# Optimization experiments

Measured on AMD Instinct MI355X. Metric: run time of the kernel, lower is better.

Reference implementation:

```python
import jax, jax.numpy as jnp
import numpy as np

B, T, I, H = 256, 512, 64, 256


def _lstm_layer(x, Wih, Whh, bih, bhh):
    # x: [B, T, in], Wih: [4H, in], Whh: [4H, H], biases: [4H]
    # PyTorch gate order: i, f, g, o.  c' = f*c + i*g ; h = o*tanh(c')
    Hd = Whh.shape[1]
    xp = jnp.einsum('bti,gi->btg', x, Wih) + bih + bhh  # [B, T, 4H]
    h0 = jnp.zeros((x.shape[0], Hd), x.dtype)
    c0 = jnp.zeros((x.shape[0], Hd), x.dtype)

    def step(carry, xt):
        h, c = carry
        g = xt + h @ Whh.T
        i, f, gg, o = jnp.split(g, 4, axis=-1)
        i = jax.nn.sigmoid(i)
        f = jax.nn.sigmoid(f)
        gg = jnp.tanh(gg)
        o = jax.nn.sigmoid(o)
        c = f * c + i * gg
        h = o * jnp.tanh(c)
        return (h, c), h

    _, hs = jax.lax.scan(step, (h0, c0), jnp.swapaxes(xp, 0, 1))  # [T, B, H]
    return jnp.swapaxes(hs, 0, 1)


def setup_inputs() -> dict:
    key = jax.random.key(0)
    ks = jax.random.split(key, 20)
    s_in = 1.0 / np.sqrt(I)
    s_h = 1.0 / np.sqrt(H)
    d = {
        'x': jax.random.normal(ks[0], (B, T, I), jnp.float32),
        # encoder layer 0: input I -> H
        'enc_Wih0': jax.random.normal(ks[1], (4 * H, I), jnp.float32) * s_in,
        'enc_Whh0': jax.random.normal(ks[2], (4 * H, H), jnp.float32) * s_h,
        'enc_bih0': jnp.zeros((4 * H,), jnp.float32),
        'enc_bhh0': jnp.zeros((4 * H,), jnp.float32),
        # encoder layer 1: H -> H
        'enc_Wih1': jax.random.normal(ks[3], (4 * H, H), jnp.float32) * s_h,
        'enc_Whh1': jax.random.normal(ks[4], (4 * H, H), jnp.float32) * s_h,
        'enc_bih1': jnp.zeros((4 * H,), jnp.float32),
        'enc_bhh1': jnp.zeros((4 * H,), jnp.float32),
        # decoder layer 0: H -> H
        'dec_Wih0': jax.random.normal(ks[5], (4 * H, H), jnp.float32) * s_h,
        'dec_Whh0': jax.random.normal(ks[6], (4 * H, H), jnp.float32) * s_h,
        'dec_bih0': jnp.zeros((4 * H,), jnp.float32),
        'dec_bhh0': jnp.zeros((4 * H,), jnp.float32),
        # decoder layer 1: H -> H
        'dec_Wih1': jax.random.normal(ks[7], (4 * H, H), jnp.float32) * s_h,
        'dec_Whh1': jax.random.normal(ks[8], (4 * H, H), jnp.float32) * s_h,
        'dec_bih1': jnp.zeros((4 * H,), jnp.float32),
        'dec_bhh1': jnp.zeros((4 * H,), jnp.float32),
        # output projection H -> I
        'out_W': jax.random.normal(ks[9], (I, H), jnp.float32) * s_h,
        'out_b': jnp.zeros((I,), jnp.float32),
    }
    return d


def reference(x,
              enc_Wih0, enc_Whh0, enc_bih0, enc_bhh0,
              enc_Wih1, enc_Whh1, enc_bih1, enc_bhh1,
              dec_Wih0, dec_Whh0, dec_bih0, dec_bhh0,
              dec_Wih1, dec_Whh1, dec_bih1, dec_bhh1,
              out_W, out_b):
    # Encoder (2 stacked LSTM layers, inference mode -> no inter-layer dropout)
    h = _lstm_layer(x, enc_Wih0, enc_Whh0, enc_bih0, enc_bhh0)
    encoded = _lstm_layer(h, enc_Wih1, enc_Whh1, enc_bih1, enc_bhh1)
    # Decoder (2 stacked LSTM layers over the encoded sequence)
    h = _lstm_layer(encoded, dec_Wih0, dec_Whh0, dec_bih0, dec_bhh0)
    decoded_hidden = _lstm_layer(h, dec_Wih1, dec_Whh1, dec_bih1, dec_bhh1)
    # Linear projection back to input_size
    reconstruction = jnp.einsum('bth,ih->bti', decoded_hidden, out_W) + out_b
    return reconstruction
```

## Files before the change

### kernel.cpp

```cpp
#include <hip/hip_runtime.h>

typedef unsigned short u16;
typedef unsigned int   u32;
typedef _Float16 f16;
typedef _Float16 half2v __attribute__((ext_vector_type(2)));
typedef _Float16 half8v __attribute__((ext_vector_type(8)));
typedef float float4v __attribute__((ext_vector_type(4)));

#define B_  256
#define T_  512
#define I_  64
#define H_  256
#define G_  1024
#define BT_ (B_*T_)

static __device__ __forceinline__ float fdot2u(u32 a, u32 b, float c) {
#if defined(__has_builtin) && __has_builtin(__builtin_amdgcn_fdot2)
  return __builtin_amdgcn_fdot2(__builtin_bit_cast(half2v, a),
                                __builtin_bit_cast(half2v, b), c, false);
#else
  half2v av = __builtin_bit_cast(half2v, a), bv = __builtin_bit_cast(half2v, b);
  return c + (float)av.x * (float)bv.x + (float)av.y * (float)bv.y;
#endif
}

static __device__ __forceinline__ float sig_(float x) {
  return 1.0f / (1.0f + __expf(-x));
}
static __device__ __forceinline__ float tanh_(float x) {
  float ax = fminf(fabsf(x), 15.0f);
  float e  = __expf(2.0f * ax);
  float t  = (e - 1.0f) / (e + 1.0f);
  return copysignf(t, x);
}


__global__ void cvt_f16(const float* __restrict__ in, u16* __restrict__ out, int n) {
  int i = blockIdx.x * blockDim.x + threadIdx.x;
  if (i < n) out[i] = __builtin_bit_cast(u16, (f16)in[i]);
}

__global__ void split_w(const float* __restrict__ w, u16* __restrict__ hi,
                        u16* __restrict__ lo, int n) {
  int i = blockIdx.x * blockDim.x + threadIdx.x;
  if (i < n) {
    float v = w[i];
    f16 h = (f16)v;
    float r = v - (float)h;
    hi[i] = __builtin_bit_cast(u16, h);
    lo[i] = __builtin_bit_cast(u16, (f16)r);
  }
}

__global__ void bias_sum(const float* __restrict__ a, const float* __restrict__ b,
                         float* __restrict__ o, int n) {
  int i = blockIdx.x * blockDim.x + threadIdx.x;
  if (i < n) o[i] = a[i] + b[i];
}

template<int BN>
__global__ __launch_bounds__(256) void gemm_ws(
    const u16* __restrict__ A, const u16* __restrict__ Bh, const u16* __restrict__ Bl,
    const float* __restrict__ bias, float* __restrict__ C,
    int K, int tcl, int t0, int N)
{
  constexpr int BM = 128, BK = 64, LDT = 72;
  __shared__ u16 As[BM * LDT];
  __shared__ u16 Bhs[BN * LDT];
  __shared__ u16 Bls[BN * LDT];
  const int tid = threadIdx.x, wave = tid >> 6, lane = tid & 63;
  const int m0 = blockIdx.x * BM, n0 = blockIdx.y * BN;
  constexpr int WNT = BN / 32;
  const int wm0 = (wave >> 1) * 64, wn0 = (wave & 1) * (BN / 2);
  const int tcmask = (1 << tcl) - 1;
  float4v acc[4][WNT];
  for (int i = 0; i < 4; i++)
    for (int j = 0; j < WNT; j++) acc[i][j] = (float4v){0.f, 0.f, 0.f, 0.f};
  const int lrow = lane & 15, lk = (lane >> 4) * 8;

  for (int k0 = 0; k0 < K; k0 += BK) {
    __syncthreads();
#pragma unroll
    for (int i = 0; i < 4; i++) {
      int idx = tid + i * 256, row = idx >> 3, u = idx & 7;
      int m = m0 + row;
      int rg = (m >> tcl) * T_ + t0 + (m & tcmask);
      *(uint4*)(As + row * LDT + u * 8) =
          *(const uint4*)(A + (size_t)rg * K + k0 + u * 8);
    }
#pragma unroll
    for (int i = 0; i < WNT; i++) {
      int idx = tid + i * 256, row = idx >> 3, u = idx & 7;
      size_t go = (size_t)(n0 + row) * K + k0 + u * 8;
      *(uint4*)(Bhs + row * LDT + u * 8) = *(const uint4*)(Bh + go);
      *(uint4*)(Bls + row * LDT + u * 8) = *(const uint4*)(Bl + go);
    }
    __syncthreads();
#pragma unroll
    for (int ks = 0; ks < 2; ++ks) {
      int col = ks * 32 + lk;
      half8v af[4];
#pragma unroll
      for (int mt = 0; mt < 4; mt++)
        af[mt] = *(const half8v*)(const void*)(As + (wm0 + mt * 16 + lrow) * LDT + col);
#pragma unroll
      for (int nt = 0; nt < WNT; nt++) {
        half8v bhv = *(const half8v*)(const void*)(Bhs + (wn0 + nt * 16 + lrow) * LDT + col);
        half8v blv = *(const half8v*)(const void*)(Bls + (wn0 + nt * 16 + lrow) * LDT + col);
#pragma unroll
        for (int mt = 0; mt < 4; mt++) {
          acc[mt][nt] = __builtin_amdgcn_mfma_f32_16x16x32_f16(af[mt], bhv, acc[mt][nt], 0, 0, 0);
          acc[mt][nt] = __builtin_amdgcn_mfma_f32_16x16x32_f16(af[mt], blv, acc[mt][nt], 0, 0, 0);
        }
      }
    }
  }
  const int crow = (lane >> 4) * 4, ccol = lane & 15;
#pragma unroll
  for (int nt = 0; nt < WNT; nt++) {
    int n = n0 + wn0 + nt * 16 + ccol;
    float bv = bias[n];
#pragma unroll
    for (int mt = 0; mt < 4; mt++) {
#pragma unroll
      for (int r = 0; r < 4; r++) {
        int m = m0 + wm0 + mt * 16 + crow + r;
        C[(size_t)m * N + n] = acc[mt][nt][r] + bv;
      }
    }
  }
}

__global__ __launch_bounds__(512) __attribute__((amdgpu_waves_per_eu(2, 2)))
void lstm_scan(
    const u16* __restrict__ whh, const float* __restrict__ xp,
    u16* __restrict__ hout, float* __restrict__ cst, u16* __restrict__ hst,
    int Tc, int t0)
{
  __shared__ u16 wt[8 * 1024 * 8];
  __shared__ u32 hbuf[2][128];
  const int tid = threadIdx.x, b = blockIdx.x;
  const int lane = tid & 63, wv = tid >> 6;
  const int u = wv * 32 + (lane & 31);
  const int g0 = lane >> 5;
  const int r0 = g0 * 256 + u;
  const int r1 = (g0 + 2) * 256 + u;

  uint4 w0[24], w1[24];
  {
    const uint4* gp0 = (const uint4*)(whh + (size_t)r0 * 256);
    const uint4* gp1 = (const uint4*)(whh + (size_t)r1 * 256);
#pragma unroll
    for (int i = 0; i < 24; i++) { w0[i] = gp0[i]; w1[i] = gp1[i]; }
#pragma unroll
    for (int q = 0; q < 8; q++) {
      *(uint4*)(wt + (size_t)(q * 1024 + r0) * 8) = gp0[24 + q];
      *(uint4*)(wt + (size_t)(q * 1024 + r1) * 8) = gp1[24 + q];
    }
  }

  float cc = 0.f;
  if (t0 == 0) {
    if (tid < 128) hbuf[0][tid] = 0u;
  } else {
    cc = cst[(size_t)b * 256 + u];
    if (tid < 128) hbuf[0][tid] = ((const u32*)hst)[(size_t)b * 128 + tid];
  }
  __syncthreads();

  const float* xpb = xp + (size_t)b * Tc * 1024;
  float xn0 = xpb[r0], xn1 = xpb[r1];
  u16* houtb = hout + ((size_t)b * T_ + t0) * 256;

  u16 hb = 0;
  for (int tt = 0; tt < Tc; ++tt) {
    float a0 = xn0, a1 = xn1;
    if (tt + 1 < Tc) {
      xn0 = xpb[(size_t)(tt + 1) * 1024 + r0];
      xn1 = xpb[(size_t)(tt + 1) * 1024 + r1];
    }
    const uint4* hq = (const uint4*)hbuf[tt & 1];
#pragma unroll
    for (int kc = 0; kc < 24; ++kc) {
      uint4 hv = hq[kc];
      a0 = fdot2u(w0[kc].x, hv.x, a0); a0 = fdot2u(w0[kc].y, hv.y, a0);
      a0 = fdot2u(w0[kc].z, hv.z, a0); a0 = fdot2u(w0[kc].w, hv.w, a0);
      a1 = fdot2u(w1[kc].x, hv.x, a1); a1 = fdot2u(w1[kc].y, hv.y, a1);
      a1 = fdot2u(w1[kc].z, hv.z, a1); a1 = fdot2u(w1[kc].w, hv.w, a1);
    }
#pragma unroll
    for (int q = 0; q < 8; ++q) {
      uint4 hv = hq[24 + q];
      uint4 t0v = *(const uint4*)(wt + (size_t)(q * 1024 + r0) * 8);
      uint4 t1v = *(const uint4*)(wt + (size_t)(q * 1024 + r1) * 8);
      a0 = fdot2u(t0v.x, hv.x, a0); a0 = fdot2u(t0v.y, hv.y, a0);
      a0 = fdot2u(t0v.z, hv.z, a0); a0 = fdot2u(t0v.w, hv.w, a0);
      a1 = fdot2u(t1v.x, hv.x, a1); a1 = fdot2u(t1v.y, hv.y, a1);
      a1 = fdot2u(t1v.z, hv.z, a1); a1 = fdot2u(t1v.w, hv.w, a1);
    }
    float b0 = __shfl_xor(a0, 32);
    float b1 = __shfl_xor(a1, 32);
    float ipre = g0 ? b0 : a0;
    float fpre = g0 ? a0 : b0;
    float gpre = g0 ? b1 : a1;
    float opre = g0 ? a1 : b1;
    float iv = sig_(ipre), fv = sig_(fpre), gv = tanh_(gpre), ov = sig_(opre);
    cc = fv * cc + iv * gv;
    float hval = ov * tanh_(cc);
    hb = __builtin_bit_cast(u16, (f16)hval);
    if (g0 == 0) {
      ((u16*)hbuf[(tt + 1) & 1])[u] = hb;
      houtb[(size_t)tt * 256 + u] = hb;
    }
    __syncthreads();
  }
  if (g0 == 0) {
    cst[(size_t)b * 256 + u] = cc;
    hst[(size_t)b * 256 + u] = hb;
  }
}


extern "C" void kernel_launch(void* const* d_in, const int* in_sizes, int n_in,
                              void* d_out, int out_size, void* d_ws, size_t ws_size,
                              hipStream_t stream)
{
  const float* x      = (const float*)d_in[0];
  const float* Wih[4] = {(const float*)d_in[1], (const float*)d_in[5],
                         (const float*)d_in[9], (const float*)d_in[13]};
  const float* Whh[4] = {(const float*)d_in[2], (const float*)d_in[6],
                         (const float*)d_in[10], (const float*)d_in[14]};
  const float* bi[4]  = {(const float*)d_in[3], (const float*)d_in[7],
                         (const float*)d_in[11], (const float*)d_in[15]};
  const float* bh[4]  = {(const float*)d_in[4], (const float*)d_in[8],
                         (const float*)d_in[12], (const float*)d_in[16]};
  const float* outW   = (const float*)d_in[17];
  const float* outb   = (const float*)d_in[18];

  char* ws = (char*)d_ws;
  size_t off = 0;
  auto alc = [&](size_t bytes) -> char* {
    char* p = ws + off;
    off = (off + bytes + 255) & ~(size_t)255;
    return p;
  };

  u16* xf  = (u16*)alc((size_t)BT_ * I_ * 2);
  u16* hb0 = (u16*)alc((size_t)BT_ * H_ * 2);
  u16* hb1 = (u16*)alc((size_t)BT_ * H_ * 2);
  int wihn[4] = {G_ * I_, G_ * H_, G_ * H_, G_ * H_};
  u16 *wihH[4], *wihL[4], *whhH[4];
  float* bsum[4];
  for (int l = 0; l < 4; l++) {
    wihH[l] = (u16*)alc((size_t)wihn[l] * 2);
    wihL[l] = (u16*)alc((size_t)wihn[l] * 2);
    whhH[l] = (u16*)alc((size_t)G_ * H_ * 2);
    bsum[l] = (float*)alc((size_t)G_ * 4);
  }
  u16* owH = (u16*)alc((size_t)I_ * H_ * 2);
  u16* owL = (u16*)alc((size_t)I_ * H_ * 2);
  float* cst = (float*)alc((size_t)B_ * H_ * 4);
  u16*   hst = (u16*)alc((size_t)B_ * H_ * 2);

  int Tc = T_;
  while (Tc > 16 && off + (size_t)B_ * Tc * G_ * 4 + 4096 > ws_size) Tc >>= 1;
  float* xpb = (float*)alc((size_t)B_ * Tc * G_ * 4);
  int tcl = 0;
  while ((1 << tcl) < Tc) tcl++;

  {
    int n = BT_ * I_;
    cvt_f16<<<dim3((n + 255) / 256), dim3(256), 0, stream>>>(x, xf, n);
  }
  for (int l = 0; l < 4; l++) {
    split_w<<<dim3((wihn[l] + 255) / 256), dim3(256), 0, stream>>>(Wih[l], wihH[l], wihL[l], wihn[l]);
    cvt_f16<<<dim3((G_ * H_ + 255) / 256), dim3(256), 0, stream>>>(Whh[l], whhH[l], G_ * H_);
    bias_sum<<<dim3(4), dim3(256), 0, stream>>>(bi[l], bh[l], bsum[l], G_);
  }
  split_w<<<dim3((I_ * H_ + 255) / 256), dim3(256), 0, stream>>>(outW, owH, owL, I_ * H_);

  for (int l = 0; l < 4; l++) {
    const u16* Ain = (l == 0) ? xf : ((l == 1) ? hb0 : (l == 2) ? hb1 : hb0);
    u16* Hout = (l & 1) ? hb1 : hb0;
    int K = (l == 0) ? I_ : H_;
    for (int t0 = 0; t0 < T_; t0 += Tc) {
      gemm_ws<128><<<dim3((B_ * Tc) / 128, G_ / 128), dim3(256), 0, stream>>>(
          Ain, wihH[l], wihL[l], bsum[l], xpb, K, tcl, t0, G_);
      lstm_scan<<<dim3(B_), dim3(512), 0, stream>>>(whhH[l], xpb, Hout, cst, hst, Tc, t0);
    }
  }

  gemm_ws<64><<<dim3(BT_ / 128, 1), dim3(256), 0, stream>>>(
      hb1, owH, owL, outb, (float*)d_out, H_, 9, 0, I_);
}
```

Measured before the change: 5.279 ms.

## Pin recurrent weights in AGPRs and broadcast hidden state via readlane

Stores the register-resident W_hh slice in accumulation registers (AGPRs) through inline-asm pinning and copies it back to VGPRs at use. This frees VGPRs and drops the waves_per_eu constraint. For the first 16 chunks, the hidden state is loaded once per lane and broadcast with readlane instead of repeated LDS vector loads, which cuts LDS traffic on the serial recurrence. The cost is extra AGPR-to-VGPR moves and scalar readlane instructions on every timestep, and the inline-asm constraints may not steer register allocation as intended.

```diff
diff --git a/kernel.cpp b/kernel.cpp
--- a/kernel.cpp
+++ b/kernel.cpp
@@ -13,6 +13,9 @@
 #define H_  256
 #define G_  1024
 #define BT_ (B_*T_)
+
+#define AG_PIN(dst, src) asm volatile("" : "=a"(dst) : "0"(src))
+#define AG_GET(dst, src) asm volatile("" : "=v"(dst) : "0"(src))
 
 static __device__ __forceinline__ float fdot2u(u32 a, u32 b, float c) {
 #if defined(__has_builtin) && __has_builtin(__builtin_amdgcn_fdot2)
@@ -131,8 +134,7 @@
   }
 }
 
-__global__ __launch_bounds__(512) __attribute__((amdgpu_waves_per_eu(2, 2)))
-void lstm_scan(
+__global__ __launch_bounds__(512) void lstm_scan(
     const u16* __restrict__ whh, const float* __restrict__ xp,
     u16* __restrict__ hout, float* __restrict__ cst, u16* __restrict__ hst,
     int Tc, int t0)
@@ -146,12 +148,16 @@
   const int r0 = g0 * 256 + u;
   const int r1 = (g0 + 2) * 256 + u;
 
-  uint4 w0[24], w1[24];
+  float4v wA[48];
   {
     const uint4* gp0 = (const uint4*)(whh + (size_t)r0 * 256);
     const uint4* gp1 = (const uint4*)(whh + (size_t)r1 * 256);
 #pragma unroll
-    for (int i = 0; i < 24; i++) { w0[i] = gp0[i]; w1[i] = gp1[i]; }
+    for (int i = 0; i < 24; i++) {
+      uint4 q0 = gp0[i], q1 = gp1[i];
+      AG_PIN(wA[i],      __builtin_bit_cast(float4v, q0));
+      AG_PIN(wA[24 + i], __builtin_bit_cast(float4v, q1));
+    }
 #pragma unroll
     for (int q = 0; q < 8; q++) {
       *(uint4*)(wt + (size_t)(q * 1024 + r0) * 8) = gp0[24 + q];
@@ -179,14 +185,38 @@
       xn0 = xpb[(size_t)(tt + 1) * 1024 + r0];
       xn1 = xpb[(size_t)(tt + 1) * 1024 + r1];
     }
-    const uint4* hq = (const uint4*)hbuf[tt & 1];
-#pragma unroll
-    for (int kc = 0; kc < 24; ++kc) {
+    const u32* hcur = hbuf[tt & 1];
+    u32 hg = hcur[lane];
+    const uint4* hq = (const uint4*)hcur;
+
+#pragma unroll
+    for (int kc = 0; kc < 16; ++kc) {
+      float4v q0, q1;
+      AG_GET(q0, wA[kc]);
+      AG_GET(q1, wA[24 + kc]);
+      uint4 w0 = __builtin_bit_cast(uint4, q0);
+      uint4 w1 = __builtin_bit_cast(uint4, q1);
+      u32 h0 = __builtin_amdgcn_readlane(hg, 4 * kc + 0);
+      u32 h1 = __builtin_amdgcn_readlane(hg, 4 * kc + 1);
+      u32 h2 = __builtin_amdgcn_readlane(hg, 4 * kc + 2);
+      u32 h3 = __builtin_amdgcn_readlane(hg, 4 * kc + 3);
+      a0 = fdot2u(w0.x, h0, a0); a0 = fdot2u(w0.y, h1, a0);
+      a0 = fdot2u(w0.z, h2, a0); a0 = fdot2u(w0.w, h3, a0);
+      a1 = fdot2u(w1.x, h0, a1); a1 = fdot2u(w1.y, h1, a1);
+      a1 = fdot2u(w1.z, h2, a1); a1 = fdot2u(w1.w, h3, a1);
+    }
+#pragma unroll
+    for (int kc = 16; kc < 24; ++kc) {
+      float4v q0, q1;
+      AG_GET(q0, wA[kc]);
+      AG_GET(q1, wA[24 + kc]);
+      uint4 w0 = __builtin_bit_cast(uint4, q0);
+      uint4 w1 = __builtin_bit_cast(uint4, q1);
       uint4 hv = hq[kc];
-      a0 = fdot2u(w0[kc].x, hv.x, a0); a0 = fdot2u(w0[kc].y, hv.y, a0);
-      a0 = fdot2u(w0[kc].z, hv.z, a0); a0 = fdot2u(w0[kc].w, hv.w, a0);
-      a1 = fdot2u(w1[kc].x, hv.x, a1); a1 = fdot2u(w1[kc].y, hv.y, a1);
-      a1 = fdot2u(w1[kc].z, hv.z, a1); a1 = fdot2u(w1[kc].w, hv.w, a1);
+      a0 = fdot2u(w0.x, hv.x, a0); a0 = fdot2u(w0.y, hv.y, a0);
+      a0 = fdot2u(w0.z, hv.z, a0); a0 = fdot2u(w0.w, hv.w, a0);
+      a1 = fdot2u(w1.x, hv.x, a1); a1 = fdot2u(w1.y, hv.y, a1);
+      a1 = fdot2u(w1.z, hv.z, a1); a1 = fdot2u(w1.w, hv.w, a1);
     }
 #pragma unroll
     for (int q = 0; q < 8; ++q) {
```

New measurement: 7.700 ms. 45.9% more time.

## Broadcast hidden state via readlane and move one more weight chunk to LDS

Applied to the files above, without the earlier changes.

The recurrent matvec in the LSTM scan no longer reads the hidden state from LDS as uint4 broadcasts each step. Instead each wave loads the 128 packed h words into two VGPRs and broadcasts them to scalar registers with readlane. One more 16-byte weight chunk per row moves from registers to LDS (23 in registers, 9 in LDS), which lowers register pressure. The main loop is marked not to unroll, and the xp prefetch is made unconditional by clamping the index. The aim is to cut LDS read traffic and free registers, at the cost of many readlane/SALU instructions and extra LDS weight reads on the critical serial path.

```diff
diff --git a/kernel.cpp b/kernel.cpp
--- a/kernel.cpp
+++ b/kernel.cpp
@@ -131,13 +131,14 @@
   }
 }
 
-__global__ __launch_bounds__(512) __attribute__((amdgpu_waves_per_eu(2, 2)))
+__global__ __attribute__((amdgpu_flat_work_group_size(512, 512),
+                          amdgpu_waves_per_eu(2, 2)))
 void lstm_scan(
     const u16* __restrict__ whh, const float* __restrict__ xp,
     u16* __restrict__ hout, float* __restrict__ cst, u16* __restrict__ hst,
     int Tc, int t0)
 {
-  __shared__ u16 wt[8 * 1024 * 8];
+  __shared__ u16 wt[9 * 1024 * 8];
   __shared__ u32 hbuf[2][128];
   const int tid = threadIdx.x, b = blockIdx.x;
   const int lane = tid & 63, wv = tid >> 6;
@@ -146,25 +147,29 @@
   const int r0 = g0 * 256 + u;
   const int r1 = (g0 + 2) * 256 + u;
 
-  uint4 w0[24], w1[24];
   {
     const uint4* gp0 = (const uint4*)(whh + (size_t)r0 * 256);
     const uint4* gp1 = (const uint4*)(whh + (size_t)r1 * 256);
 #pragma unroll
-    for (int i = 0; i < 24; i++) { w0[i] = gp0[i]; w1[i] = gp1[i]; }
-#pragma unroll
-    for (int q = 0; q < 8; q++) {
-      *(uint4*)(wt + (size_t)(q * 1024 + r0) * 8) = gp0[24 + q];
-      *(uint4*)(wt + (size_t)(q * 1024 + r1) * 8) = gp1[24 + q];
-    }
-  }
-
+    for (int q = 0; q < 9; q++) {
+      *(uint4*)(wt + (q * 1024 + r0) * 8) = gp0[23 + q];
+      *(uint4*)(wt + (q * 1024 + r1) * 8) = gp1[23 + q];
+    }
+  }
   float cc = 0.f;
   if (t0 == 0) {
     if (tid < 128) hbuf[0][tid] = 0u;
   } else {
-    cc = cst[(size_t)b * 256 + u];
-    if (tid < 128) hbuf[0][tid] = ((const u32*)hst)[(size_t)b * 128 + tid];
+    cc = cst[b * 256 + u];
+    if (tid < 128) hbuf[0][tid] = ((const u32*)hst)[b * 128 + tid];
+  }
+
+  uint4 wr0[23], wr1[23];
+  {
+    const uint4* gp0 = (const uint4*)(whh + (size_t)r0 * 256);
+    const uint4* gp1 = (const uint4*)(whh + (size_t)r1 * 256);
+#pragma unroll
+    for (int i = 0; i < 23; i++) { wr0[i] = gp0[i]; wr1[i] = gp1[i]; }
   }
   __syncthreads();
 
@@ -173,30 +178,44 @@
   u16* houtb = hout + ((size_t)b * T_ + t0) * 256;
 
   u16 hb = 0;
+#pragma clang loop unroll(disable)
   for (int tt = 0; tt < Tc; ++tt) {
     float a0 = xn0, a1 = xn1;
-    if (tt + 1 < Tc) {
-      xn0 = xpb[(size_t)(tt + 1) * 1024 + r0];
-      xn1 = xpb[(size_t)(tt + 1) * 1024 + r1];
-    }
-    const uint4* hq = (const uint4*)hbuf[tt & 1];
-#pragma unroll
-    for (int kc = 0; kc < 24; ++kc) {
-      uint4 hv = hq[kc];
-      a0 = fdot2u(w0[kc].x, hv.x, a0); a0 = fdot2u(w0[kc].y, hv.y, a0);
-      a0 = fdot2u(w0[kc].z, hv.z, a0); a0 = fdot2u(w0[kc].w, hv.w, a0);
-      a1 = fdot2u(w1[kc].x, hv.x, a1); a1 = fdot2u(w1[kc].y, hv.y, a1);
-      a1 = fdot2u(w1[kc].z, hv.z, a1); a1 = fdot2u(w1[kc].w, hv.w, a1);
-    }
-#pragma unroll
-    for (int q = 0; q < 8; ++q) {
-      uint4 hv = hq[24 + q];
-      uint4 t0v = *(const uint4*)(wt + (size_t)(q * 1024 + r0) * 8);
-      uint4 t1v = *(const uint4*)(wt + (size_t)(q * 1024 + r1) * 8);
-      a0 = fdot2u(t0v.x, hv.x, a0); a0 = fdot2u(t0v.y, hv.y, a0);
-      a0 = fdot2u(t0v.z, hv.z, a0); a0 = fdot2u(t0v.w, hv.w, a0);
-      a1 = fdot2u(t1v.x, hv.x, a1); a1 = fdot2u(t1v.y, hv.y, a1);
-      a1 = fdot2u(t1v.z, hv.z, a1); a1 = fdot2u(t1v.w, hv.w, a1);
+    {
+      int ttn = (tt + 1 < Tc) ? (tt + 1) : tt;
+      xn0 = xpb[ttn * 1024 + r0];
+      xn1 = xpb[ttn * 1024 + r1];
+    }
+    const u32* hcur = hbuf[tt & 1];
+    u32 hg0 = hcur[lane];
+    u32 hg1 = hcur[64 + lane];
+
+#pragma unroll
+    for (int qi = 0; qi < 32; ++qi) {
+      u32 h0, h1, h2, h3;
+      if (qi < 16) {
+        h0 = __builtin_amdgcn_readlane(hg0, 4 * qi + 0);
+        h1 = __builtin_amdgcn_readlane(hg0, 4 * qi + 1);
+        h2 = __builtin_amdgcn_readlane(hg0, 4 * qi + 2);
+        h3 = __builtin_amdgcn_readlane(hg0, 4 * qi + 3);
+      } else {
+        h0 = __builtin_amdgcn_readlane(hg1, 4 * qi - 64);
+        h1 = __builtin_amdgcn_readlane(hg1, 4 * qi - 63);
+        h2 = __builtin_amdgcn_readlane(hg1, 4 * qi - 62);
+        h3 = __builtin_amdgcn_readlane(hg1, 4 * qi - 61);
+      }
+      uint4 w0, w1;
+      if (qi < 23) {
+        w0 = wr0[qi];
+        w1 = wr1[qi];
+      } else {
+        w0 = *(const uint4*)(wt + ((qi - 23) * 1024 + r0) * 8);
+        w1 = *(const uint4*)(wt + ((qi - 23) * 1024 + r1) * 8);
+      }
+      a0 = fdot2u(w0.x, h0, a0); a0 = fdot2u(w0.y, h1, a0);
+      a0 = fdot2u(w0.z, h2, a0); a0 = fdot2u(w0.w, h3, a0);
+      a1 = fdot2u(w1.x, h0, a1); a1 = fdot2u(w1.y, h1, a1);
+      a1 = fdot2u(w1.z, h2, a1); a1 = fdot2u(w1.w, h3, a1);
     }
     float b0 = __shfl_xor(a0, 32);
     float b1 = __shfl_xor(a1, 32);
@@ -210,13 +229,13 @@
     hb = __builtin_bit_cast(u16, (f16)hval);
     if (g0 == 0) {
       ((u16*)hbuf[(tt + 1) & 1])[u] = hb;
-      houtb[(size_t)tt * 256 + u] = hb;
+      houtb[tt * 256 + u] = hb;
     }
     __syncthreads();
   }
   if (g0 == 0) {
-    cst[(size_t)b * 256 + u] = cc;
-    hst[(size_t)b * 256 + u] = hb;
+    cst[b * 256 + u] = cc;
+    hst[b * 256 + u] = hb;
   }
 }
 
```

New measurement: 5.648 ms. 7.0% more time.
